# Optimization experiments

Measured on AMD Instinct MI355X. Metric: run time of the kernel, lower is better.

The kernel has to match this reference:

```python
import jax, jax.numpy as jnp
import numpy as np

INPUT_DIM = 2048
NUM_EXPERTS = 64
TOP_K = 2


def setup_inputs() -> dict:
    key = jax.random.key(0)
    kx, kw, kb = jax.random.split(key, 3)
    x = jax.random.normal(kx, (4, 4096, INPUT_DIM), dtype=jnp.float32)
    # nn.Linear default init: U(-1/sqrt(fan_in), 1/sqrt(fan_in))
    bound = 1.0 / np.sqrt(INPUT_DIM)
    W = jax.random.uniform(kw, (INPUT_DIM, NUM_EXPERTS), dtype=jnp.float32, minval=-bound, maxval=bound)
    b = jax.random.uniform(kb, (NUM_EXPERTS,), dtype=jnp.float32, minval=-bound, maxval=bound)
    return {"x": x, "W": W, "b": b}


def reference(x, W, b):
    # router_logits = Linear(x); p = softmax(logits, -1); topk over experts
    logits = jnp.einsum("bsd,de->bse", x, W) + b          # [B, S, E]
    p = jax.nn.softmax(logits, axis=-1)                     # [B, S, E]
    gate_vals, expert_idx = jax.lax.top_k(p, TOP_K)         # [B, S, k] each
    return expert_idx, gate_vals
```

## Files before the change

### kernel.cpp

```cpp
#include <hip/hip_runtime.h>
#include <hip/hip_bf16.h>
#include <math.h>


#define DIM 2048
#define NE 64

typedef __attribute__((ext_vector_type(8))) short short8;
typedef __attribute__((ext_vector_type(4))) float floatx4;

__device__ __forceinline__ short bf16bits(float v) {
  __hip_bfloat16 h = __float2bfloat16(v);
  return *(short*)&h;
}
__device__ __forceinline__ float bf16tof(short s) {
  unsigned int u = ((unsigned int)(unsigned short)s) << 16;
  union { unsigned int u; float f; } c; c.u = u;
  return c.f;
}

__global__ void wprep_kernel(const float* __restrict__ W, short8* __restrict__ wf) {
  const int s = blockIdx.x >> 2, n = blockIdx.x & 3, l = threadIdx.x;
  const int d0 = s * 32 + (l >> 4) * 8;
  const int e = n * 16 + (l & 15);
  short8 vh, vl;
#pragma unroll
  for (int j = 0; j < 8; ++j) {
    float v = W[(size_t)(d0 + j) * NE + e];
    short h = bf16bits(v);
    vh[j] = h;
    vl[j] = bf16bits(v - bf16tof(h));
  }
  wf[(size_t)((s * 4 + n) * 2 + 0) * 64 + l] = vh;
  wf[(size_t)((s * 4 + n) * 2 + 1) * 64 + l] = vl;
}

__device__ __forceinline__ void async_copy16(const float* g, void* lds) {
  __builtin_amdgcn_global_load_lds(
      (const __attribute__((address_space(1))) unsigned int*)g,
      (__attribute__((address_space(3))) unsigned int*)lds, 16, 0, 0);
}

__global__ __launch_bounds__(256, 2) void router_main(
    const float* __restrict__ x, const short8* __restrict__ wf,
    const float* __restrict__ b, float* __restrict__ out, int ntok) {
  __shared__ alignas(16) char smem[65536];
  const int tid = threadIdx.x;
  const int lane = tid & 63;
  const int kq = tid >> 6;
  const int tok0 = blockIdx.x * 32;
  const int r4 = lane >> 4;
  const int g = lane & 15;

  char* mybuf = smem + kq * 16384;
  const float* xbase = x + (size_t)tok0 * DIM + kq * 512;

  floatx4 acc[2][4];
#pragma unroll
  for (int mt = 0; mt < 2; ++mt)
#pragma unroll
    for (int n = 0; n < 4; ++n) acc[mt][n] = (floatx4){0.f, 0.f, 0.f, 0.f};

  auto issue = [&](int c, int sel) {
    const float* gb = xbase + c * 64;
    char* dst = mybuf + sel * 8192;
#pragma unroll
    for (int p = 0; p < 8; ++p) {
      const int rr = p * 4 + r4;
      const float* gp = gb + (size_t)rr * DIM + (((g + rr) & 15) << 2);
      async_copy16(gp, dst + p * 1024);
    }
  };

  issue(0, 0);
  __syncthreads();

  for (int c = 0; c < 8; ++c) {
    if (c < 7) issue(c + 1, (c + 1) & 1);
    const float* bb = (const float*)(mybuf + (c & 1) * 8192);
#pragma unroll
    for (int u = 0; u < 2; ++u) {
      const int sg = kq * 16 + c * 2 + u;
      const short8* wp = wf + (size_t)sg * 8 * 64;
      short8 Wh[4], Wl[4];
#pragma unroll
      for (int n = 0; n < 4; ++n) {
        Wh[n] = wp[(n * 2 + 0) * 64 + lane];
        Wl[n] = wp[(n * 2 + 1) * 64 + lane];
      }
#pragma unroll
      for (int mt = 0; mt < 2; ++mt) {
        const int rr = mt * 16 + g;
        const int G0 = u * 8 + r4 * 2;
        floatx4 a0 = *(const floatx4*)(bb + rr * 64 + (((G0 - rr) & 15) << 2));
        floatx4 a1 = *(const floatx4*)(bb + rr * 64 + (((G0 + 1 - rr) & 15) << 2));
        short8 Ah, Al;
#pragma unroll
        for (int j = 0; j < 4; ++j) {
          short h = bf16bits(a0[j]);
          Ah[j] = h; Al[j] = bf16bits(a0[j] - bf16tof(h));
        }
#pragma unroll
        for (int j = 0; j < 4; ++j) {
          short h = bf16bits(a1[j]);
          Ah[4 + j] = h; Al[4 + j] = bf16bits(a1[j] - bf16tof(h));
        }
#pragma unroll
        for (int n = 0; n < 4; ++n) {
          acc[mt][n] = __builtin_amdgcn_mfma_f32_16x16x32_bf16(Ah, Wh[n], acc[mt][n], 0, 0, 0);
          acc[mt][n] = __builtin_amdgcn_mfma_f32_16x16x32_bf16(Ah, Wl[n], acc[mt][n], 0, 0, 0);
          acc[mt][n] = __builtin_amdgcn_mfma_f32_16x16x32_bf16(Al, Wh[n], acc[mt][n], 0, 0, 0);
        }
      }
    }
    __syncthreads();
  }

  float* red = (float*)smem;
  float* lgt = (float*)(smem + 33792);
#pragma unroll
  for (int mt = 0; mt < 2; ++mt)
#pragma unroll
    for (int n = 0; n < 4; ++n)
#pragma unroll
      for (int r = 0; r < 4; ++r) {
        const int tokl = mt * 16 + r4 * 4 + r;
        const int e = n * 16 + g;
        red[(kq * 32 + tokl) * 66 + e] = acc[mt][n][r];
      }
  __syncthreads();

  if (tid < 32) {
    const int t = tid;
    float v1 = -INFINITY, v2 = -INFINITY;
    int i1 = 0, i2 = 0;
#pragma unroll 8
    for (int e = 0; e < 64; ++e) {
      float v = red[t * 66 + e] + red[(32 + t) * 66 + e] +
                red[(64 + t) * 66 + e] + red[(96 + t) * 66 + e] + b[e];
      lgt[t * 65 + e] = v;
      if (v > v1) { v2 = v1; i2 = i1; v1 = v; i1 = e; }
      else if (v > v2) { v2 = v; i2 = e; }
    }
    float s = 0.f;
#pragma unroll 8
    for (int e = 0; e < 64; ++e) s += __expf(lgt[t * 65 + e] - v1);
    const int tok = tok0 + t;
    out[tok * 2 + 0] = (float)i1;
    out[tok * 2 + 1] = (float)i2;
    out[ntok * 2 + tok * 2 + 0] = 1.0f / s;
    out[ntok * 2 + tok * 2 + 1] = __expf(v2 - v1) / s;
  }
}

extern "C" void kernel_launch(void* const* d_in, const int* in_sizes, int n_in,
                              void* d_out, int out_size, void* d_ws, size_t ws_size,
                              hipStream_t stream) {
  const float* x = (const float*)d_in[0];
  const float* W = (const float*)d_in[1];
  const float* b = (const float*)d_in[2];
  float* out = (float*)d_out;
  const int ntok = in_sizes[0] / DIM;
  short8* wf = (short8*)d_ws;

  wprep_kernel<<<256, 64, 0, stream>>>(W, wf);
  router_main<<<ntok / 32, 256, 0, stream>>>(x, wf, b, out, ntok);
}
```

Measured before the change: 203.8 us.

## Shrink per-wave LDS staging, drop per-chunk block barriers, parallelize top-k epilogue

Each wave now stages 32-column chunks in a smaller private double buffer, cutting LDS from 64KB to about 33KB and raising launch bounds to 3 blocks per CU. Per-chunk __syncthreads are replaced by a wave-local s_waitcnt vmcnt, since each wave only reads its own buffer. The softmax/top-2 epilogue now runs on all 256 threads, with shuffle-based reductions instead of 32 serial threads. The aim is more occupancy and less barrier stall; correctness relies on vmcnt(4) covering the W loads and async LDS copies in the right order.

```diff
diff --git a/kernel.cpp b/kernel.cpp
--- a/kernel.cpp
+++ b/kernel.cpp
@@ -14,8 +14,8 @@
   return *(short*)&h;
 }
 __device__ __forceinline__ float bf16tof(short s) {
-  unsigned int u = ((unsigned int)(unsigned short)s) << 16;
-  union { unsigned int u; float f; } c; c.u = u;
+  union { unsigned int u; float f; } c;
+  c.u = ((unsigned int)(unsigned short)s) << 16;
   return c.f;
 }
 
@@ -41,19 +41,28 @@
       (__attribute__((address_space(3))) unsigned int*)lds, 16, 0, 0);
 }
 
-__global__ __launch_bounds__(256, 2) void router_main(
+__global__ __launch_bounds__(256, 3) void router_main(
     const float* __restrict__ x, const short8* __restrict__ wf,
     const float* __restrict__ b, float* __restrict__ out, int ntok) {
-  __shared__ alignas(16) char smem[65536];
+  __shared__ alignas(16) char smem[33280];
   const int tid = threadIdx.x;
   const int lane = tid & 63;
   const int kq = tid >> 6;
+  const int g = lane & 15, r4 = lane >> 4;
   const int tok0 = blockIdx.x * 32;
-  const int r4 = lane >> 4;
-  const int g = lane & 15;
 
-  char* mybuf = smem + kq * 16384;
-  const float* xbase = x + (size_t)tok0 * DIM + kq * 512;
+  char* mybuf = smem + kq * 8192;
+  const float* xb = x + (size_t)tok0 * DIM + kq * 512;
+
+  auto issue = [&](int c, char* dst) {
+    const float* gb = xb + c * 32;
+#pragma unroll
+    for (int p = 0; p < 4; ++p) {
+      const int rr = p * 8 + (lane >> 3);
+      const float* gp = gb + (size_t)rr * DIM + ((((lane & 7) - rr) & 7) << 2);
+      async_copy16(gp, dst + p * 1024);
+    }
+  };
 
   floatx4 acc[2][4];
 #pragma unroll
@@ -61,63 +70,49 @@
 #pragma unroll
     for (int n = 0; n < 4; ++n) acc[mt][n] = (floatx4){0.f, 0.f, 0.f, 0.f};
 
-  auto issue = [&](int c, int sel) {
-    const float* gb = xbase + c * 64;
-    char* dst = mybuf + sel * 8192;
+  issue(0, mybuf);
+
+  for (int c = 0; c < 16; ++c) {
+    const int sg = kq * 16 + c;
+    const short8* wp = wf + (size_t)sg * 8 * 64;
+    short8 Wh[4], Wl[4];
 #pragma unroll
-    for (int p = 0; p < 8; ++p) {
-      const int rr = p * 4 + r4;
-      const float* gp = gb + (size_t)rr * DIM + (((g + rr) & 15) << 2);
-      async_copy16(gp, dst + p * 1024);
+    for (int n = 0; n < 4; ++n) {
+      Wh[n] = wp[(n * 2 + 0) * 64 + lane];
+      Wl[n] = wp[(n * 2 + 1) * 64 + lane];
     }
-  };
+    if (c < 15) issue(c + 1, mybuf + ((c + 1) & 1) * 4096);
+    asm volatile("s_waitcnt vmcnt(4)" ::: "memory");
 
-  issue(0, 0);
-  __syncthreads();
-
-  for (int c = 0; c < 8; ++c) {
-    if (c < 7) issue(c + 1, (c + 1) & 1);
-    const float* bb = (const float*)(mybuf + (c & 1) * 8192);
+    const float* bb = (const float*)(mybuf + (c & 1) * 4096);
 #pragma unroll
-    for (int u = 0; u < 2; ++u) {
-      const int sg = kq * 16 + c * 2 + u;
-      const short8* wp = wf + (size_t)sg * 8 * 64;
-      short8 Wh[4], Wl[4];
+    for (int mt = 0; mt < 2; ++mt) {
+      const int row = mt * 16 + g;
+      const int ga0 = r4 * 2;
+      floatx4 a0 = *(const floatx4*)(bb + row * 32 + (((ga0 + 0 + row) & 7) << 2));
+      floatx4 a1 = *(const floatx4*)(bb + row * 32 + (((ga0 + 1 + row) & 7) << 2));
+      short8 Ah, Al;
+#pragma unroll
+      for (int j = 0; j < 4; ++j) {
+        short h = bf16bits(a0[j]);
+        Ah[j] = h; Al[j] = bf16bits(a0[j] - bf16tof(h));
+      }
+#pragma unroll
+      for (int j = 0; j < 4; ++j) {
+        short h = bf16bits(a1[j]);
+        Ah[4 + j] = h; Al[4 + j] = bf16bits(a1[j] - bf16tof(h));
+      }
 #pragma unroll
       for (int n = 0; n < 4; ++n) {
-        Wh[n] = wp[(n * 2 + 0) * 64 + lane];
-        Wl[n] = wp[(n * 2 + 1) * 64 + lane];
-      }
-#pragma unroll
-      for (int mt = 0; mt < 2; ++mt) {
-        const int rr = mt * 16 + g;
-        const int G0 = u * 8 + r4 * 2;
-        floatx4 a0 = *(const floatx4*)(bb + rr * 64 + (((G0 - rr) & 15) << 2));
-        floatx4 a1 = *(const floatx4*)(bb + rr * 64 + (((G0 + 1 - rr) & 15) << 2));
-        short8 Ah, Al;
-#pragma unroll
-        for (int j = 0; j < 4; ++j) {
-          short h = bf16bits(a0[j]);
-          Ah[j] = h; Al[j] = bf16bits(a0[j] - bf16tof(h));
-        }
-#pragma unroll
-        for (int j = 0; j < 4; ++j) {
-          short h = bf16bits(a1[j]);
-          Ah[4 + j] = h; Al[4 + j] = bf16bits(a1[j] - bf16tof(h));
-        }
-#pragma unroll
-        for (int n = 0; n < 4; ++n) {
-          acc[mt][n] = __builtin_amdgcn_mfma_f32_16x16x32_bf16(Ah, Wh[n], acc[mt][n], 0, 0, 0);
-          acc[mt][n] = __builtin_amdgcn_mfma_f32_16x16x32_bf16(Ah, Wl[n], acc[mt][n], 0, 0, 0);
-          acc[mt][n] = __builtin_amdgcn_mfma_f32_16x16x32_bf16(Al, Wh[n], acc[mt][n], 0, 0, 0);
-        }
+        acc[mt][n] = __builtin_amdgcn_mfma_f32_16x16x32_bf16(Ah, Wh[n], acc[mt][n], 0, 0, 0);
+        acc[mt][n] = __builtin_amdgcn_mfma_f32_16x16x32_bf16(Ah, Wl[n], acc[mt][n], 0, 0, 0);
+        acc[mt][n] = __builtin_amdgcn_mfma_f32_16x16x32_bf16(Al, Wh[n], acc[mt][n], 0, 0, 0);
       }
     }
-    __syncthreads();
   }
 
+  __syncthreads();
   float* red = (float*)smem;
-  float* lgt = (float*)(smem + 33792);
 #pragma unroll
   for (int mt = 0; mt < 2; ++mt)
 #pragma unroll
@@ -126,30 +121,49 @@
       for (int r = 0; r < 4; ++r) {
         const int tokl = mt * 16 + r4 * 4 + r;
         const int e = n * 16 + g;
-        red[(kq * 32 + tokl) * 66 + e] = acc[mt][n][r];
+        red[(kq * 32 + tokl) * 65 + e] = acc[mt][n][r];
       }
   __syncthreads();
 
-  if (tid < 32) {
-    const int t = tid;
+  {
+    const int tl = lane & 7, er = lane >> 3;
+    const int t = kq * 8 + tl;
+    float lv[8];
     float v1 = -INFINITY, v2 = -INFINITY;
     int i1 = 0, i2 = 0;
-#pragma unroll 8
-    for (int e = 0; e < 64; ++e) {
-      float v = red[t * 66 + e] + red[(32 + t) * 66 + e] +
-                red[(64 + t) * 66 + e] + red[(96 + t) * 66 + e] + b[e];
-      lgt[t * 65 + e] = v;
+#pragma unroll
+    for (int i = 0; i < 8; ++i) {
+      const int e = er * 8 + i;
+      float v = red[t * 65 + e] + red[(32 + t) * 65 + e] +
+                red[(64 + t) * 65 + e] + red[(96 + t) * 65 + e] + b[e];
+      lv[i] = v;
       if (v > v1) { v2 = v1; i2 = i1; v1 = v; i1 = e; }
       else if (v > v2) { v2 = v; i2 = e; }
     }
+#pragma unroll
+    for (int off = 8; off < 64; off <<= 1) {
+      float ov1 = __shfl_xor(v1, off, 64); int oi1 = __shfl_xor(i1, off, 64);
+      float ov2 = __shfl_xor(v2, off, 64); int oi2 = __shfl_xor(i2, off, 64);
+      bool aw = (v1 > ov1) || (v1 == ov1 && i1 < oi1);
+      float nv1 = aw ? v1 : ov1; int ni1 = aw ? i1 : oi1;
+      float c2v = aw ? ov1 : v1; int c2i = aw ? oi1 : i1;
+      float w2v = aw ? v2 : ov2; int w2i = aw ? i2 : oi2;
+      bool sw = (w2v > c2v) || (w2v == c2v && w2i < c2i);
+      v2 = sw ? w2v : c2v; i2 = sw ? w2i : c2i;
+      v1 = nv1; i1 = ni1;
+    }
     float s = 0.f;
-#pragma unroll 8
-    for (int e = 0; e < 64; ++e) s += __expf(lgt[t * 65 + e] - v1);
-    const int tok = tok0 + t;
-    out[tok * 2 + 0] = (float)i1;
-    out[tok * 2 + 1] = (float)i2;
-    out[ntok * 2 + tok * 2 + 0] = 1.0f / s;
-    out[ntok * 2 + tok * 2 + 1] = __expf(v2 - v1) / s;
+#pragma unroll
+    for (int i = 0; i < 8; ++i) s += __expf(lv[i] - v1);
+#pragma unroll
+    for (int off = 8; off < 64; off <<= 1) s += __shfl_xor(s, off, 64);
+    if (er == 0) {
+      const int tok = tok0 + t;
+      out[tok * 2 + 0] = (float)i1;
+      out[tok * 2 + 1] = (float)i2;
+      out[ntok * 2 + tok * 2 + 0] = 1.0f / s;
+      out[ntok * 2 + tok * 2 + 1] = __expf(v2 - v1) / s;
+    }
   }
 }
 
```

New measurement: 199.2 us. 1.02x faster.
